# Optimization experiments

Hardware: AMD Instinct MI355X
Metric: run time of the kernel (lower is better)

## Reference

```python
import jax, jax.numpy as jnp
import numpy as np

H, D = 8, 16          # heads, per-head dim (hidden 128 = H*D)
IN_C, HID, OUT_C = 128, 128, 64
NG, ND = 100000, 50000
EG, EDG = 800000, 800000
NEG_SLOPE = 0.2


def setup_inputs() -> dict:
    key = jax.random.key(0)
    ks = jax.random.split(key, 20)
    inp = {}
    inp['x_gene'] = jax.random.normal(ks[0], (NG, IN_C), jnp.float32)
    inp['x_disease'] = jax.random.normal(ks[1], (ND, IN_C), jnp.float32)
    inp['eg_src'] = jax.random.randint(ks[2], (EG,), 0, NG, jnp.int32)
    inp['eg_dst'] = jax.random.randint(ks[3], (EG,), 0, NG, jnp.int32)
    inp['edg_src'] = jax.random.randint(ks[4], (EDG,), 0, ND, jnp.int32)
    inp['edg_dst'] = jax.random.randint(ks[5], (EDG,), 0, NG, jnp.int32)
    s = 1.0 / np.sqrt(IN_C)
    inp['W_gene'] = jax.random.normal(ks[6], (IN_C, HID), jnp.float32) * s
    inp['b_gene'] = jnp.zeros((HID,), jnp.float32)
    inp['W_dis'] = jax.random.normal(ks[7], (IN_C, HID), jnp.float32) * s
    inp['b_dis'] = jnp.zeros((HID,), jnp.float32)
    inp['att_src_gg'] = jax.random.normal(ks[8], (H, D), jnp.float32) * 0.1
    inp['att_dst_gg'] = jax.random.normal(ks[9], (H, D), jnp.float32) * 0.1
    inp['att_src_dg'] = jax.random.normal(ks[10], (H, D), jnp.float32) * 0.1
    inp['att_dst_dg'] = jax.random.normal(ks[11], (H, D), jnp.float32) * 0.1
    inp['Wk'] = jax.random.normal(ks[12], (HID, HID), jnp.float32) * (1.0 / np.sqrt(HID))
    inp['bk'] = jnp.zeros((HID,), jnp.float32)
    inp['q'] = jax.random.normal(ks[13], (HID,), jnp.float32) * 0.1
    inp['W_lin'] = jax.random.normal(ks[14], (HID, OUT_C), jnp.float32) * (1.0 / np.sqrt(HID))
    inp['b_lin'] = jnp.zeros((OUT_C,), jnp.float32)
    return inp


def _edge_attn(xs, xd, src, dst, a_s, a_d, n_dst):
    # xs:[Ns,H,D] projected src feats, xd:[Nd,H,D]; GAT-style per-edge-type attention
    e_src = (xs * a_s).sum(-1)                      # [Ns,H]
    e_dst = (xd * a_d).sum(-1)                      # [Nd,H]
    alpha = jax.nn.leaky_relu(e_src[src] + e_dst[dst], NEG_SLOPE)   # [E,H]
    m = jax.ops.segment_max(alpha, dst, num_segments=n_dst)
    m = jnp.where(jnp.isfinite(m), m, 0.0)
    ex = jnp.exp(alpha - m[dst])
    denom = jax.ops.segment_sum(ex, dst, num_segments=n_dst)
    w = ex / (denom[dst] + 1e-16)                   # softmax over incoming edges
    msg = xs[src] * w[..., None]                    # [E,H,D]
    out = jax.ops.segment_sum(msg, dst, num_segments=n_dst)  # [Nd,H,D]
    return jax.nn.relu(out.reshape(n_dst, H * D))


def reference(x_gene, x_disease, eg_src, eg_dst, edg_src, edg_dst,
              W_gene, b_gene, W_dis, b_dis,
              att_src_gg, att_dst_gg, att_src_dg, att_dst_dg,
              Wk, bk, q, W_lin, b_lin):
    ng = x_gene.shape[0]
    hg = (x_gene @ W_gene + b_gene).reshape(ng, H, D)
    hd = (x_disease @ W_dis + b_dis).reshape(-1, H, D)
    # metapath aggregations landing on 'gene'
    out_gg = _edge_attn(hg, hg, eg_src, eg_dst, att_src_gg, att_dst_gg, ng)
    out_dg = _edge_attn(hd, hg, edg_src, edg_dst, att_src_dg, att_dst_dg, ng)
    outs = jnp.stack([out_gg, out_dg])              # [K=2, Ng, HID]
    # semantic-level attention
    score = (jnp.tanh(outs @ Wk + bk).mean(1) * q).sum(-1)   # [K]
    beta = jax.nn.softmax(score)
    gene = (beta[:, None, None] * outs).sum(0)      # [Ng, HID]
    return gene @ W_lin + b_lin                     # [Ng, OUT_C]
```

## Files before the change

kernel.cpp:

```cpp
#include <hip/hip_runtime.h>
#include <cstdint>
#include <cstddef>

#define NEG_SLOPE 0.2f
#define BSHIFT 8

__device__ __forceinline__ float leakyf(float x) { return x > 0.f ? x : NEG_SLOPE * x; }
__device__ __forceinline__ float fast_tanh(float x) {
    float e = __expf(2.f * x);
    return 1.f - 2.f / (e + 1.f);
}

__global__ __launch_bounds__(256) void proj_kernel(
    const float* __restrict__ x, const float* __restrict__ W, const float* __restrict__ bias,
    float* __restrict__ hout, int N,
    const float* __restrict__ att0, float* __restrict__ e0,
    const float* __restrict__ att1, float* __restrict__ e1,
    const float* __restrict__ att2, float* __restrict__ e2)
{
    __shared__ float xlds[32 * 128];
    __shared__ float wlds[16 * 128];
    const int t = threadIdx.x;
    const int row0 = blockIdx.x * 32;
    #pragma unroll
    for (int p = 0; p < 4; ++p) {
        int idx = t + 256 * p;
        int r = idx >> 5;
        int c4 = idx & 31;
        float4 v = make_float4(0.f, 0.f, 0.f, 0.f);
        if (row0 + r < N) v = *(const float4*)(x + (size_t)(row0 + r) * 128 + c4 * 4);
        *(float4*)(xlds + r * 128 + c4 * 4) = v;
    }
    const int rg = t >> 5, ct = t & 31;
    float acc[4][4];
    {
        float4 bv = *(const float4*)(bias + ct * 4);
        #pragma unroll
        for (int rr = 0; rr < 4; ++rr) {
            acc[rr][0] = bv.x; acc[rr][1] = bv.y; acc[rr][2] = bv.z; acc[rr][3] = bv.w;
        }
    }
    for (int kc = 0; kc < 8; ++kc) {
        __syncthreads();
        #pragma unroll
        for (int p = 0; p < 2; ++p) {
            int idx = t + 256 * p;
            *(float4*)(wlds + idx * 4) = *(const float4*)(W + (size_t)kc * 2048 + idx * 4);
        }
        __syncthreads();
        #pragma unroll 2
        for (int i2 = 0; i2 < 16; i2 += 4) {
            const int i = kc * 16 + i2;
            float4 xv[4];
            #pragma unroll
            for (int rr = 0; rr < 4; ++rr) xv[rr] = *(const float4*)(xlds + (rg + 8 * rr) * 128 + i);
            #pragma unroll
            for (int qq = 0; qq < 4; ++qq) {
                float4 wv = *(const float4*)(wlds + (i2 + qq) * 128 + ct * 4);
                #pragma unroll
                for (int rr = 0; rr < 4; ++rr) {
                    float xs = ((const float*)&xv[rr])[qq];
                    acc[rr][0] = fmaf(xs, wv.x, acc[rr][0]);
                    acc[rr][1] = fmaf(xs, wv.y, acc[rr][1]);
                    acc[rr][2] = fmaf(xs, wv.z, acc[rr][2]);
                    acc[rr][3] = fmaf(xs, wv.w, acc[rr][3]);
                }
            }
        }
    }
    #pragma unroll
    for (int rr = 0; rr < 4; ++rr) {
        int grow = row0 + rg + 8 * rr;
        if (grow < N)
            *(float4*)(hout + (size_t)grow * 128 + ct * 4) =
                make_float4(acc[rr][0], acc[rr][1], acc[rr][2], acc[rr][3]);
    }
    const int head = ct >> 2;
    const bool wlane = (ct & 3) == 0;
    if (att0) {
        float4 av = *(const float4*)(att0 + ct * 4);
        #pragma unroll
        for (int rr = 0; rr < 4; ++rr) {
            float p_ = acc[rr][0] * av.x + acc[rr][1] * av.y + acc[rr][2] * av.z + acc[rr][3] * av.w;
            p_ += __shfl_xor(p_, 1);
            p_ += __shfl_xor(p_, 2);
            int grow = row0 + rg + 8 * rr;
            if (wlane && grow < N) e0[(size_t)grow * 8 + head] = p_;
        }
    }
    if (att1) {
        float4 av = *(const float4*)(att1 + ct * 4);
        #pragma unroll
        for (int rr = 0; rr < 4; ++rr) {
            float p_ = acc[rr][0] * av.x + acc[rr][1] * av.y + acc[rr][2] * av.z + acc[rr][3] * av.w;
            p_ += __shfl_xor(p_, 1);
            p_ += __shfl_xor(p_, 2);
            int grow = row0 + rg + 8 * rr;
            if (wlane && grow < N) e1[(size_t)grow * 8 + head] = p_;
        }
    }
    if (att2) {
        float4 av = *(const float4*)(att2 + ct * 4);
        #pragma unroll
        for (int rr = 0; rr < 4; ++rr) {
            float p_ = acc[rr][0] * av.x + acc[rr][1] * av.y + acc[rr][2] * av.z + acc[rr][3] * av.w;
            p_ += __shfl_xor(p_, 1);
            p_ += __shfl_xor(p_, 2);
            int grow = row0 + rg + 8 * rr;
            if (wlane && grow < N) e2[(size_t)grow * 8 + head] = p_;
        }
    }
}


__global__ __launch_bounds__(256) void bucket_hist(
    const int* __restrict__ dstg, int Eg, const int* __restrict__ dstd, int Ed,
    int NBg, int NBtot, int* __restrict__ bucketCnt)
{
    __shared__ int h[1024];
    const int t = threadIdx.x;
    for (int j = t; j < NBtot; j += 256) h[j] = 0;
    __syncthreads();
    const int Etot = Eg + Ed;
    const int base = blockIdx.x * 4096;
    #pragma unroll
    for (int k = 0; k < 16; ++k) {
        int i = base + k * 256 + t;
        if (i < Etot) {
            int b = (i < Eg) ? (dstg[i] >> BSHIFT) : NBg + (dstd[i - Eg] >> BSHIFT);
            atomicAdd(&h[b], 1);
        }
    }
    __syncthreads();
    for (int j = t; j < NBtot; j += 256) {
        int c = h[j];
        if (c) atomicAdd(&bucketCnt[j], c);
    }
}

__global__ void bucket_scan(const int* __restrict__ bucketCnt, int NBtot, int Etot,
                            int* __restrict__ bucketBase, int* __restrict__ bucketCursor)
{
    __shared__ int s[1024];
    int t = threadIdx.x;
    int v = (t < NBtot) ? bucketCnt[t] : 0;
    s[t] = v;
    __syncthreads();
    for (int o = 1; o < 1024; o <<= 1) {
        int add = (t >= o) ? s[t - o] : 0;
        __syncthreads();
        s[t] += add;
        __syncthreads();
    }
    if (t < NBtot) {
        int e = s[t] - v;
        bucketBase[t] = e;
        bucketCursor[t] = e;
    }
    if (t == 0) bucketBase[NBtot] = Etot;
}

__global__ __launch_bounds__(256) void bucket_scatter(
    const int* __restrict__ dstg, const int* __restrict__ srcg, int Eg,
    const int* __restrict__ dstd, const int* __restrict__ srcd, int Ed,
    int NBg, int NBtot, int* __restrict__ bucketCursor, unsigned* __restrict__ coarse)
{
    __shared__ int h[800];
    __shared__ int basearr[800];
    __shared__ int cur[800];
    const int t = threadIdx.x;
    for (int j = t; j < NBtot; j += 256) h[j] = 0;
    __syncthreads();
    const int Etot = Eg + Ed;
    const int base = blockIdx.x * 4096;
    int bk[16];
    unsigned pk[16];
    #pragma unroll
    for (int k = 0; k < 16; ++k) {
        int i = base + k * 256 + t;
        bk[k] = -1;
        if (i < Etot) {
            int dst, src, goff;
            if (i < Eg) { dst = dstg[i]; src = srcg[i]; goff = 0; }
            else        { dst = dstd[i - Eg]; src = srcd[i - Eg]; goff = NBg; }
            bk[k] = goff + (dst >> BSHIFT);
            pk[k] = (unsigned)src | ((unsigned)(dst & 255) << 24);
            atomicAdd(&h[bk[k]], 1);
        }
    }
    __syncthreads();
    for (int j = t; j < NBtot; j += 256) {
        int c = h[j];
        basearr[j] = c ? atomicAdd(&bucketCursor[j], c) : 0;
        cur[j] = 0;
    }
    __syncthreads();
    #pragma unroll
    for (int k = 0; k < 16; ++k) {
        if (bk[k] >= 0) {
            int r = atomicAdd(&cur[bk[k]], 1);
            coarse[basearr[bk[k]] + r] = pk[k];
        }
    }
}

__global__ __launch_bounds__(256) void bucket_sort(
    const unsigned* __restrict__ coarse, const int* __restrict__ bucketBase,
    int NBg, int Eg, int Ed, int N,
    int* __restrict__ offg, int* __restrict__ offd,
    int* __restrict__ srcs_g, int* __restrict__ srcs_d)
{
    __shared__ int hist[256];
    __shared__ int excl[256];
    __shared__ int cur[256];
    const int b = blockIdx.x;
    const int t = threadIdx.x;
    const int s0 = bucketBase[b], s1 = bucketBase[b + 1];
    const int cnt = s1 - s0;
    const bool isg = b < NBg;
    const int d0 = (isg ? b : b - NBg) << BSHIFT;
    hist[t] = 0;
    __syncthreads();
    for (int i = t; i < cnt; i += 256) {
        unsigned p = coarse[s0 + i];
        atomicAdd(&hist[p >> 24], 1);
    }
    __syncthreads();
    int v = hist[t];
    excl[t] = v;
    __syncthreads();
    for (int o = 1; o < 256; o <<= 1) {
        int add = (t >= o) ? excl[t - o] : 0;
        __syncthreads();
        excl[t] += add;
        __syncthreads();
    }
    const int e = excl[t] - v;
    const int localBase = isg ? s0 : s0 - Eg;
    const int d = d0 + t;
    if (d < N) {
        if (isg) offg[d] = localBase + e;
        else     offd[d] = localBase + e;
    }
    cur[t] = e;
    __syncthreads();
    int* outp = isg ? srcs_g : srcs_d;
    for (int i = t; i < cnt; i += 256) {
        unsigned p = coarse[s0 + i];
        int r = atomicAdd(&cur[p >> 24], 1);
        outp[localBase + r] = (int)(p & 0xFFFFFFu);
    }
    if (b == 0 && t == 0) { offg[N] = Eg; offd[N] = Ed; }
}

__global__ __launch_bounds__(256) void aggregate_kernel(
    const float* __restrict__ xs,
    const float* __restrict__ esrc,
    const float* __restrict__ edst,
    const int* __restrict__ off,
    const int* __restrict__ srcsorted,
    float* __restrict__ outp,
    int Nd)
{
    __shared__ float exbuf[4][64 * 8];
    const int lane = threadIdx.x & 63;
    const int wslot = threadIdx.x >> 6;
    const int n = blockIdx.x * 4 + wslot;
    if (n >= Nd) return;
    const int o0 = off[n], o1 = off[n + 1];
    const int deg = o1 - o0;
    const int li = lane & 31, half = lane >> 5;
    const int j0 = li * 4;
    const int hh = li >> 2;
    if (deg == 0) {
        if (half == 0) *(float4*)(outp + (size_t)n * 128 + j0) = make_float4(0.f, 0.f, 0.f, 0.f);
        return;
    }
    float ed[8];
    {
        float4 a = *(const float4*)(edst + (size_t)n * 8);
        float4 b = *(const float4*)(edst + (size_t)n * 8 + 4);
        ed[0] = a.x; ed[1] = a.y; ed[2] = a.z; ed[3] = a.w;
        ed[4] = b.x; ed[5] = b.y; ed[6] = b.z; ed[7] = b.w;
    }
    if (deg <= 64) {
        const bool act = lane < deg;
        int s = act ? srcsorted[o0 + lane] : 0;
        float m[8];
        {
            float4 ea = make_float4(0.f, 0.f, 0.f, 0.f), eb = ea;
            if (act) {
                ea = *(const float4*)(esrc + (size_t)s * 8);
                eb = *(const float4*)(esrc + (size_t)s * 8 + 4);
            }
            float a[8] = {ea.x, ea.y, ea.z, ea.w, eb.x, eb.y, eb.z, eb.w};
            #pragma unroll
            for (int h2 = 0; h2 < 8; ++h2) m[h2] = act ? leakyf(a[h2] + ed[h2]) : -1e30f;
        }
        float al[8];
        #pragma unroll
        for (int h2 = 0; h2 < 8; ++h2) al[h2] = m[h2];
        for (int o = 1; o < deg; o <<= 1) {
            #pragma unroll
            for (int h2 = 0; h2 < 8; ++h2) m[h2] = fmaxf(m[h2], __shfl_xor(m[h2], o));
        }
        float exv[8];
        #pragma unroll
        for (int h2 = 0; h2 < 8; ++h2) exv[h2] = act ? __expf(al[h2] - m[h2]) : 0.f;
        *(float4*)(&exbuf[wslot][lane * 8])     = make_float4(exv[0], exv[1], exv[2], exv[3]);
        *(float4*)(&exbuf[wslot][lane * 8 + 4]) = make_float4(exv[4], exv[5], exv[6], exv[7]);
        float4 num = make_float4(0.f, 0.f, 0.f, 0.f);
        float den = 0.f;
        const int iters = (deg + 1) >> 1;
        #pragma unroll 2
        for (int k = 0; k < iters; ++k) {
            int i = 2 * k + half;
            if (i < deg) {
                int si = __shfl(s, i);
                float wgt = exbuf[wslot][i * 8 + hh];
                float4 xv = *(const float4*)(xs + (size_t)si * 128 + j0);
                num.x = fmaf(wgt, xv.x, num.x);
                num.y = fmaf(wgt, xv.y, num.y);
                num.z = fmaf(wgt, xv.z, num.z);
                num.w = fmaf(wgt, xv.w, num.w);
                den += wgt;
            }
        }
        num.x += __shfl_xor(num.x, 32);
        num.y += __shfl_xor(num.y, 32);
        num.z += __shfl_xor(num.z, 32);
        num.w += __shfl_xor(num.w, 32);
        den += __shfl_xor(den, 32);
        if (half == 0) {
            float inv = 1.f / (den + 1e-16f);
            float4 r;
            r.x = fmaxf(num.x * inv, 0.f);
            r.y = fmaxf(num.y * inv, 0.f);
            r.z = fmaxf(num.z * inv, 0.f);
            r.w = fmaxf(num.w * inv, 0.f);
            *(float4*)(outp + (size_t)n * 128 + j0) = r;
        }
        return;
    }
    {
        const int j0b = lane * 2;
        const int h = lane >> 3;
        float m[8];
        #pragma unroll
        for (int hh2 = 0; hh2 < 8; ++hh2) m[hh2] = -1e30f;
        for (int base = 0; base < deg; base += 64) {
            int ii = base + lane;
            bool act = ii < deg;
            int s = srcsorted[o0 + (act ? ii : 0)];
            float4 ea = *(const float4*)(esrc + (size_t)s * 8);
            float4 eb = *(const float4*)(esrc + (size_t)s * 8 + 4);
            float a[8] = {ea.x, ea.y, ea.z, ea.w, eb.x, eb.y, eb.z, eb.w};
            #pragma unroll
            for (int hh2 = 0; hh2 < 8; ++hh2) {
                float v = act ? leakyf(a[hh2] + ed[hh2]) : -1e30f;
                #pragma unroll
                for (int o = 1; o < 64; o <<= 1) v = fmaxf(v, __shfl_xor(v, o));
                m[hh2] = fmaxf(m[hh2], v);
            }
        }
        float mh, edh;
        {
            float t4a = (h & 4) ? m[4] : m[0];
            float t4b = (h & 4) ? m[5] : m[1];
            float t4c = (h & 4) ? m[6] : m[2];
            float t4d = (h & 4) ? m[7] : m[3];
            float t2a = (h & 2) ? t4c : t4a;
            float t2b = (h & 2) ? t4d : t4b;
            mh = (h & 1) ? t2b : t2a;
            float u4a = (h & 4) ? ed[4] : ed[0];
            float u4b = (h & 4) ? ed[5] : ed[1];
            float u4c = (h & 4) ? ed[6] : ed[2];
            float u4d = (h & 4) ? ed[7] : ed[3];
            float u2a = (h & 2) ? u4c : u4a;
            float u2b = (h & 2) ? u4d : u4b;
            edh = (h & 1) ? u2b : u2a;
        }
        float den = 0.f, num0 = 0.f, num1 = 0.f;
        for (int base = 0; base < deg; base += 64) {
            int ii = base + lane;
            bool act = ii < deg;
            int sreg = srcsorted[o0 + (act ? ii : 0)];
            int cl = deg - base;
            if (cl > 64) cl = 64;
            for (int i = 0; i < cl; ++i) {
                int s = __shfl(sreg, i);
                float ev = esrc[(size_t)s * 8 + h];
                float ex = __expf(leakyf(ev + edh) - mh);
                float2 xv = *(const float2*)(xs + (size_t)s * 128 + j0b);
                num0 = fmaf(ex, xv.x, num0);
                num1 = fmaf(ex, xv.y, num1);
                den += ex;
            }
        }
        float inv = 1.f / (den + 1e-16f);
        float r0 = num0 * inv, r1 = num1 * inv;
        r0 = r0 > 0.f ? r0 : 0.f;
        r1 = r1 > 0.f ? r1 : 0.f;
        *(float2*)(outp + (size_t)n * 128 + j0b) = make_float2(r0, r1);
    }
}

__global__ __launch_bounds__(256) void score2_kernel(
    const float* __restrict__ gg, const float* __restrict__ dg,
    const float* __restrict__ Wk, const float* __restrict__ bk, const float* __restrict__ q,
    float* __restrict__ scoreAcc, int N)
{
    __shared__ float tile[32 * 128];
    __shared__ float wlds[16 * 128];
    __shared__ float sred[8];
    const int t = threadIdx.x;
    const int row0 = blockIdx.x * 16;
    #pragma unroll
    for (int p = 0; p < 4; ++p) {
        int idx = t + 256 * p;
        int r = idx >> 5;
        int c4 = idx & 31;
        int gr = row0 + (r & 15);
        const float* srcp = (r < 16) ? gg : dg;
        float4 v = make_float4(0.f, 0.f, 0.f, 0.f);
        if (gr < N) v = *(const float4*)(srcp + (size_t)gr * 128 + c4 * 4);
        *(float4*)(tile + r * 128 + c4 * 4) = v;
    }
    const int rg = t >> 5, ct = t & 31;
    float acc[4][4];
    {
        float4 bv = *(const float4*)(bk + ct * 4);
        #pragma unroll
        for (int rr = 0; rr < 4; ++rr) {
            acc[rr][0] = bv.x; acc[rr][1] = bv.y; acc[rr][2] = bv.z; acc[rr][3] = bv.w;
        }
    }
    for (int kc = 0; kc < 8; ++kc) {
        __syncthreads();
        #pragma unroll
        for (int p = 0; p < 2; ++p) {
            int idx = t + 256 * p;
            *(float4*)(wlds + idx * 4) = *(const float4*)(Wk + (size_t)kc * 2048 + idx * 4);
        }
        __syncthreads();
        #pragma unroll 2
        for (int i2 = 0; i2 < 16; i2 += 4) {
            const int i = kc * 16 + i2;
            float4 xv[4];
            #pragma unroll
            for (int rr = 0; rr < 4; ++rr) xv[rr] = *(const float4*)(tile + (rg + 8 * rr) * 128 + i);
            #pragma unroll
            for (int qq = 0; qq < 4; ++qq) {
                float4 wv = *(const float4*)(wlds + (i2 + qq) * 128 + ct * 4);
                #pragma unroll
                for (int rr = 0; rr < 4; ++rr) {
                    float xs = ((const float*)&xv[rr])[qq];
                    acc[rr][0] = fmaf(xs, wv.x, acc[rr][0]);
                    acc[rr][1] = fmaf(xs, wv.y, acc[rr][1]);
                    acc[rr][2] = fmaf(xs, wv.z, acc[rr][2]);
                    acc[rr][3] = fmaf(xs, wv.w, acc[rr][3]);
                }
            }
        }
    }
    float4 qv = *(const float4*)(q + ct * 4);
    float pg = 0.f, pd = 0.f;
    #pragma unroll
    for (int rr = 0; rr < 4; ++rr) {
        int r = rg + 8 * rr;
        int grow = row0 + (r & 15);
        if (grow < N) {
            float p_ = 0.f;
            p_ = fmaf(fast_tanh(acc[rr][0]), qv.x, p_);
            p_ = fmaf(fast_tanh(acc[rr][1]), qv.y, p_);
            p_ = fmaf(fast_tanh(acc[rr][2]), qv.z, p_);
            p_ = fmaf(fast_tanh(acc[rr][3]), qv.w, p_);
            if (r < 16) pg += p_; else pd += p_;
        }
    }
    #pragma unroll
    for (int o = 1; o < 64; o <<= 1) {
        pg += __shfl_xor(pg, o);
        pd += __shfl_xor(pd, o);
    }
    if ((t & 63) == 0) {
        sred[(t >> 6) * 2] = pg;
        sred[(t >> 6) * 2 + 1] = pd;
    }
    __syncthreads();
    if (t == 0) {
        float sg = sred[0] + sred[2] + sred[4] + sred[6];
        float sd = sred[1] + sred[3] + sred[5] + sred[7];
        int slot = blockIdx.x & 63;
        atomicAdd(&scoreAcc[slot], sg);
        atomicAdd(&scoreAcc[64 + slot], sd);
    }
}

__global__ void beta_kernel(float* __restrict__ scoreAcc, float invN) {
    int t = threadIdx.x;
    float v0 = scoreAcc[t];
    float v1 = scoreAcc[64 + t];
    #pragma unroll
    for (int o = 1; o < 64; o <<= 1) {
        v0 += __shfl_xor(v0, o);
        v1 += __shfl_xor(v1, o);
    }
    if (t == 0) {
        float s0 = v0 * invN, s1 = v1 * invN;
        float mx = fmaxf(s0, s1);
        float e0 = __expf(s0 - mx), e1 = __expf(s1 - mx);
        float inv = 1.f / (e0 + e1);
        scoreAcc[128] = e0 * inv;
        scoreAcc[129] = e1 * inv;
    }
}

__global__ __launch_bounds__(256) void final_kernel(
    const float* __restrict__ gg, const float* __restrict__ dg,
    const float* __restrict__ beta,
    const float* __restrict__ Wl, const float* __restrict__ bl,
    float* __restrict__ outp, int N)
{
    __shared__ float wlds[128 * 64];
    __shared__ float glds[32 * 128];
    const int t = threadIdx.x;
    #pragma unroll
    for (int p = 0; p < 8; ++p) {
        int idx = (t + 256 * p) * 4;
        *(float4*)(wlds + idx) = *(const float4*)(Wl + idx);
    }
    const float bet0 = beta[0], bet1 = beta[1];
    const int row0 = blockIdx.x * 32;
    #pragma unroll
    for (int p = 0; p < 4; ++p) {
        int idx = t + 256 * p;
        int r = idx >> 5;
        int c4 = idx & 31;
        float4 a = make_float4(0.f, 0.f, 0.f, 0.f), b = a, g;
        if (row0 + r < N) {
            a = *(const float4*)(gg + (size_t)(row0 + r) * 128 + c4 * 4);
            b = *(const float4*)(dg + (size_t)(row0 + r) * 128 + c4 * 4);
        }
        g.x = bet0 * a.x + bet1 * b.x;
        g.y = bet0 * a.y + bet1 * b.y;
        g.z = bet0 * a.z + bet1 * b.z;
        g.w = bet0 * a.w + bet1 * b.w;
        *(float4*)(glds + r * 128 + c4 * 4) = g;
    }
    __syncthreads();
    const int rg = t >> 5, ct = t & 31;
    float acc[4][2];
    {
        float2 bv = *(const float2*)(bl + ct * 2);
        #pragma unroll
        for (int rr = 0; rr < 4; ++rr) { acc[rr][0] = bv.x; acc[rr][1] = bv.y; }
    }
    #pragma unroll 2
    for (int i = 0; i < 128; i += 4) {
        float4 xv[4];
        #pragma unroll
        for (int rr = 0; rr < 4; ++rr) xv[rr] = *(const float4*)(glds + (rg + 8 * rr) * 128 + i);
        #pragma unroll
        for (int qq = 0; qq < 4; ++qq) {
            float2 wv = *(const float2*)(wlds + (i + qq) * 64 + ct * 2);
            #pragma unroll
            for (int rr = 0; rr < 4; ++rr) {
                float xs = ((const float*)&xv[rr])[qq];
                acc[rr][0] = fmaf(xs, wv.x, acc[rr][0]);
                acc[rr][1] = fmaf(xs, wv.y, acc[rr][1]);
            }
        }
    }
    #pragma unroll
    for (int rr = 0; rr < 4; ++rr) {
        int grow = row0 + rg + 8 * rr;
        if (grow < N)
            *(float2*)(outp + (size_t)grow * 64 + ct * 2) = make_float2(acc[rr][0], acc[rr][1]);
    }
}

extern "C" void kernel_launch(void* const* d_in, const int* in_sizes, int n_in,
                              void* d_out, int out_size, void* d_ws, size_t ws_size,
                              hipStream_t stream) {
    (void)n_in; (void)out_size; (void)ws_size;
    const float* x_gene = (const float*)d_in[0];
    const float* x_dis  = (const float*)d_in[1];
    const int* eg_src   = (const int*)d_in[2];
    const int* eg_dst   = (const int*)d_in[3];
    const int* edg_src  = (const int*)d_in[4];
    const int* edg_dst  = (const int*)d_in[5];
    const float* W_gene = (const float*)d_in[6];
    const float* b_gene = (const float*)d_in[7];
    const float* W_dis  = (const float*)d_in[8];
    const float* b_dis  = (const float*)d_in[9];
    const float* att_src_gg = (const float*)d_in[10];
    const float* att_dst_gg = (const float*)d_in[11];
    const float* att_src_dg = (const float*)d_in[12];
    const float* att_dst_dg = (const float*)d_in[13];
    const float* Wk    = (const float*)d_in[14];
    const float* bk    = (const float*)d_in[15];
    const float* q     = (const float*)d_in[16];
    const float* W_lin = (const float*)d_in[17];
    const float* b_lin = (const float*)d_in[18];
    float* out = (float*)d_out;

    const int NG_ = in_sizes[0] / 128;
    const int ND_ = in_sizes[1] / 128;
    const int EG_ = in_sizes[2];
    const int EDG_ = in_sizes[4];

    char* w = (char*)d_ws;
    auto alloc = [&](size_t bytes) -> char* {
        char* p = w;
        w += (bytes + 255) & ~(size_t)255;
        return p;
    };
    float* hg       = (float*)alloc((size_t)NG_ * 128 * 4);
    float* hd       = (float*)alloc((size_t)ND_ * 128 * 4);
    float* e_src_gg = (float*)alloc((size_t)NG_ * 8 * 4);
    float* e_dst_gg = (float*)alloc((size_t)NG_ * 8 * 4);
    float* e_dst_dg = (float*)alloc((size_t)NG_ * 8 * 4);
    float* e_src_dg = (float*)alloc((size_t)ND_ * 8 * 4);
    float* out_gg   = (float*)alloc((size_t)NG_ * 128 * 4);
    int* offg  = (int*)alloc((size_t)(NG_ + 1) * 4);
    int* offd  = (int*)alloc((size_t)(NG_ + 1) * 4);
    int* srcs_g = (int*)alloc((size_t)EG_ * 4);
    int* srcs_d = (int*)alloc((size_t)EDG_ * 4);
    unsigned* coarse = (unsigned*)alloc((size_t)(EG_ + EDG_) * 4);
    int* bucketCnt    = (int*)alloc(4096);
    int* bucketBase   = (int*)alloc(4096);
    int* bucketCursor = (int*)alloc(4096);
    float* score = (float*)alloc(1024);
    float* out_dg = hg;

    const int NBg = (NG_ + 255) >> BSHIFT;
    const int NBtot = 2 * NBg;
    const int Etot = EG_ + EDG_;
    const int nbE = (Etot + 4095) / 4096;

    proj_kernel<<<(NG_ + 31) / 32, 256, 0, stream>>>(
        x_gene, W_gene, b_gene, hg, NG_,
        att_src_gg, e_src_gg, att_dst_gg, e_dst_gg, att_dst_dg, e_dst_dg);
    proj_kernel<<<(ND_ + 31) / 32, 256, 0, stream>>>(
        x_dis, W_dis, b_dis, hd, ND_,
        att_src_dg, e_src_dg, (const float*)nullptr, (float*)nullptr,
        (const float*)nullptr, (float*)nullptr);

    hipMemsetAsync(bucketCnt, 0, (size_t)NBtot * 4, stream);
    bucket_hist<<<nbE, 256, 0, stream>>>(eg_dst, EG_, edg_dst, EDG_, NBg, NBtot, bucketCnt);
    bucket_scan<<<1, 1024, 0, stream>>>(bucketCnt, NBtot, Etot, bucketBase, bucketCursor);
    bucket_scatter<<<nbE, 256, 0, stream>>>(
        eg_dst, eg_src, EG_, edg_dst, edg_src, EDG_, NBg, NBtot, bucketCursor, coarse);
    bucket_sort<<<NBtot, 256, 0, stream>>>(
        coarse, bucketBase, NBg, EG_, EDG_, NG_, offg, offd, srcs_g, srcs_d);

    aggregate_kernel<<<(NG_ + 3) / 4, 256, 0, stream>>>(
        hg, e_src_gg, e_dst_gg, offg, srcs_g, out_gg, NG_);
    aggregate_kernel<<<(NG_ + 3) / 4, 256, 0, stream>>>(
        hd, e_src_dg, e_dst_dg, offd, srcs_d, out_dg, NG_);

    hipMemsetAsync(score, 0, 512, stream);
    score2_kernel<<<(NG_ + 15) / 16, 256, 0, stream>>>(out_gg, out_dg, Wk, bk, q, score, NG_);
    beta_kernel<<<1, 64, 0, stream>>>(score, 1.0f / (float)NG_);

    final_kernel<<<(NG_ + 31) / 32, 256, 0, stream>>>(
        out_gg, out_dg, score + 128, W_lin, b_lin, out, NG_);
}
```

Before: 427.0 us.

## Compute semantic attention scores with bf16 MFMA instead of FP32 FMA

Replaces the FP32 scalar-FMA score kernel with one that converts the 64 output rows per block (32 from each metapath) to bf16 in swizzled LDS and multiplies them by a pre-transposed bf16 Wk using 16x16x32 MFMA instructions, then applies bias, tanh and q. A small kernel transposes and converts Wk to bf16 once per call. This moves the Ng x 128 x 128 matmul onto matrix cores and halves the block count, at the cost of bf16 rounding in the score that feeds the softmax beta.

```diff
diff --git a/kernel.cpp b/kernel.cpp
--- a/kernel.cpp
+++ b/kernel.cpp
@@ -4,11 +4,19 @@
 
 #define NEG_SLOPE 0.2f
 #define BSHIFT 8
+
+typedef __attribute__((ext_vector_type(8))) short short8;
+typedef __attribute__((ext_vector_type(4))) float f32x4;
 
 __device__ __forceinline__ float leakyf(float x) { return x > 0.f ? x : NEG_SLOPE * x; }
 __device__ __forceinline__ float fast_tanh(float x) {
     float e = __expf(2.f * x);
     return 1.f - 2.f / (e + 1.f);
+}
+__device__ __forceinline__ unsigned short f2bf(float x) {
+    unsigned u = __float_as_uint(x);
+    unsigned r = u + 0x7FFFu + ((u >> 16) & 1u);
+    return (unsigned short)(r >> 16);
 }
 
 __global__ __launch_bounds__(256) void proj_kernel(
@@ -112,7 +120,6 @@
     }
 }
 
-
 __global__ __launch_bounds__(256) void bucket_hist(
     const int* __restrict__ dstg, int Eg, const int* __restrict__ dstd, int Ed,
     int NBg, int NBtot, int* __restrict__ bucketCnt)
@@ -405,95 +412,86 @@
     }
 }
 
-__global__ __launch_bounds__(256) void score2_kernel(
+__global__ void wkt_kernel(const float* __restrict__ Wk, unsigned short* __restrict__ WkT) {
+    int c = threadIdx.x;
+    for (int k = 0; k < 128; ++k)
+        WkT[c * 128 + k] = f2bf(Wk[(size_t)k * 128 + c]);
+}
+
+__global__ __launch_bounds__(256) void score2_mfma(
     const float* __restrict__ gg, const float* __restrict__ dg,
-    const float* __restrict__ Wk, const float* __restrict__ bk, const float* __restrict__ q,
+    const unsigned short* __restrict__ WkT,
+    const float* __restrict__ bk, const float* __restrict__ q,
     float* __restrict__ scoreAcc, int N)
 {
-    __shared__ float tile[32 * 128];
-    __shared__ float wlds[16 * 128];
-    __shared__ float sred[8];
+    __shared__ short atile[64 * 128];
+    __shared__ float sred[4];
     const int t = threadIdx.x;
-    const int row0 = blockIdx.x * 16;
-    #pragma unroll
-    for (int p = 0; p < 4; ++p) {
-        int idx = t + 256 * p;
-        int r = idx >> 5;
-        int c4 = idx & 31;
-        int gr = row0 + (r & 15);
-        const float* srcp = (r < 16) ? gg : dg;
-        float4 v = make_float4(0.f, 0.f, 0.f, 0.f);
-        if (gr < N) v = *(const float4*)(srcp + (size_t)gr * 128 + c4 * 4);
-        *(float4*)(tile + r * 128 + c4 * 4) = v;
-    }
-    const int rg = t >> 5, ct = t & 31;
-    float acc[4][4];
+    const int row0 = blockIdx.x * 32;
     {
-        float4 bv = *(const float4*)(bk + ct * 4);
-        #pragma unroll
-        for (int rr = 0; rr < 4; ++rr) {
-            acc[rr][0] = bv.x; acc[rr][1] = bv.y; acc[rr][2] = bv.z; acc[rr][3] = bv.w;
-        }
-    }
-    for (int kc = 0; kc < 8; ++kc) {
-        __syncthreads();
-        #pragma unroll
-        for (int p = 0; p < 2; ++p) {
-            int idx = t + 256 * p;
-            *(float4*)(wlds + idx * 4) = *(const float4*)(Wk + (size_t)kc * 2048 + idx * 4);
-        }
-        __syncthreads();
-        #pragma unroll 2
-        for (int i2 = 0; i2 < 16; i2 += 4) {
-            const int i = kc * 16 + i2;
-            float4 xv[4];
-            #pragma unroll
-            for (int rr = 0; rr < 4; ++rr) xv[rr] = *(const float4*)(tile + (rg + 8 * rr) * 128 + i);
-            #pragma unroll
-            for (int qq = 0; qq < 4; ++qq) {
-                float4 wv = *(const float4*)(wlds + (i2 + qq) * 128 + ct * 4);
-                #pragma unroll
-                for (int rr = 0; rr < 4; ++rr) {
-                    float xs = ((const float*)&xv[rr])[qq];
-                    acc[rr][0] = fmaf(xs, wv.x, acc[rr][0]);
-                    acc[rr][1] = fmaf(xs, wv.y, acc[rr][1]);
-                    acc[rr][2] = fmaf(xs, wv.z, acc[rr][2]);
-                    acc[rr][3] = fmaf(xs, wv.w, acc[rr][3]);
-                }
+        const int row = t >> 2, q4 = t & 3;
+        const int gr = row0 + (row & 31);
+        const float* srcp = (row < 32) ? gg : dg;
+        #pragma unroll
+        for (int c = 0; c < 4; ++c) {
+            const int kc = q4 * 4 + c;
+            float4 l0 = make_float4(0.f, 0.f, 0.f, 0.f), l1 = l0;
+            if (gr < N) {
+                l0 = *(const float4*)(srcp + (size_t)gr * 128 + kc * 8);
+                l1 = *(const float4*)(srcp + (size_t)gr * 128 + kc * 8 + 4);
             }
-        }
-    }
-    float4 qv = *(const float4*)(q + ct * 4);
-    float pg = 0.f, pd = 0.f;
-    #pragma unroll
-    for (int rr = 0; rr < 4; ++rr) {
-        int r = rg + 8 * rr;
-        int grow = row0 + (r & 15);
-        if (grow < N) {
-            float p_ = 0.f;
-            p_ = fmaf(fast_tanh(acc[rr][0]), qv.x, p_);
-            p_ = fmaf(fast_tanh(acc[rr][1]), qv.y, p_);
-            p_ = fmaf(fast_tanh(acc[rr][2]), qv.z, p_);
-            p_ = fmaf(fast_tanh(acc[rr][3]), qv.w, p_);
-            if (r < 16) pg += p_; else pd += p_;
-        }
-    }
-    #pragma unroll
-    for (int o = 1; o < 64; o <<= 1) {
-        pg += __shfl_xor(pg, o);
-        pd += __shfl_xor(pd, o);
-    }
-    if ((t & 63) == 0) {
-        sred[(t >> 6) * 2] = pg;
-        sred[(t >> 6) * 2 + 1] = pd;
-    }
+            int4 u;
+            u.x = (int)f2bf(l0.x) | ((int)f2bf(l0.y) << 16);
+            u.y = (int)f2bf(l0.z) | ((int)f2bf(l0.w) << 16);
+            u.z = (int)f2bf(l1.x) | ((int)f2bf(l1.y) << 16);
+            u.w = (int)f2bf(l1.z) | ((int)f2bf(l1.w) << 16);
+            const int chunk = row * 16 + kc;
+            const int chunk_sw = chunk ^ (row & 7);
+            *(int4*)((char*)atile + chunk_sw * 16) = u;
+        }
+    }
+    __syncthreads();
+    const int w = t >> 6, l = t & 63;
+    const int lrow = l & 15, lk = l >> 4;
+    f32x4 acc[8];
+    #pragma unroll
+    for (int ct = 0; ct < 8; ++ct) { acc[ct][0] = 0.f; acc[ct][1] = 0.f; acc[ct][2] = 0.f; acc[ct][3] = 0.f; }
+    #pragma unroll
+    for (int ks = 0; ks < 4; ++ks) {
+        const int rowl = w * 16 + lrow;
+        const int chunk = rowl * 16 + ks * 4 + lk;
+        const int chunk_sw = chunk ^ (rowl & 7);
+        short8 afr = *(short8*)((char*)atile + chunk_sw * 16);
+        #pragma unroll
+        for (int ct = 0; ct < 8; ++ct) {
+            const unsigned short* bp = WkT + ((size_t)(ct * 16 + lrow) * 128 + ks * 32 + lk * 8);
+            short8 bfr = *(const short8*)bp;
+            acc[ct] = __builtin_amdgcn_mfma_f32_16x16x32_bf16(afr, bfr, acc[ct], 0, 0, 0);
+        }
+    }
+    float s = 0.f;
+    #pragma unroll
+    for (int ct = 0; ct < 8; ++ct) {
+        const int col = ct * 16 + lrow;
+        const float bkv = bk[col];
+        const float qv = q[col];
+        #pragma unroll
+        for (int r = 0; r < 4; ++r) {
+            const int rloc = lk * 4 + r;
+            const int grow = row0 + ((w * 16 + rloc) & 31);
+            if (grow < N) s = fmaf(fast_tanh(acc[ct][r] + bkv), qv, s);
+        }
+    }
+    #pragma unroll
+    for (int o = 1; o < 64; o <<= 1) s += __shfl_xor(s, o);
+    if (l == 0) sred[w] = s;
     __syncthreads();
     if (t == 0) {
-        float sg = sred[0] + sred[2] + sred[4] + sred[6];
-        float sd = sred[1] + sred[3] + sred[5] + sred[7];
+        float pg = sred[0] + sred[1];
+        float pd = sred[2] + sred[3];
         int slot = blockIdx.x & 63;
-        atomicAdd(&scoreAcc[slot], sg);
-        atomicAdd(&scoreAcc[64 + slot], sd);
+        atomicAdd(&scoreAcc[slot], pg);
+        atomicAdd(&scoreAcc[64 + slot], pd);
     }
 }
 
@@ -631,6 +629,7 @@
     int* bucketCnt    = (int*)alloc(4096);
     int* bucketBase   = (int*)alloc(4096);
     int* bucketCursor = (int*)alloc(4096);
+    unsigned short* WkT = (unsigned short*)alloc(128 * 128 * 2);
     float* score = (float*)alloc(1024);
     float* out_dg = hg;
 
@@ -646,6 +645,7 @@
         x_dis, W_dis, b_dis, hd, ND_,
         att_src_dg, e_src_dg, (const float*)nullptr, (float*)nullptr,
         (const float*)nullptr, (float*)nullptr);
+    wkt_kernel<<<1, 128, 0, stream>>>(Wk, WkT);
 
     hipMemsetAsync(bucketCnt, 0, (size_t)NBtot * 4, stream);
     bucket_hist<<<nbE, 256, 0, stream>>>(eg_dst, EG_, edg_dst, EDG_, NBg, NBtot, bucketCnt);
@@ -661,7 +661,7 @@
         hd, e_src_dg, e_dst_dg, offd, srcs_d, out_dg, NG_);
 
     hipMemsetAsync(score, 0, 512, stream);
-    score2_kernel<<<(NG_ + 15) / 16, 256, 0, stream>>>(out_gg, out_dg, Wk, bk, q, score, NG_);
+    score2_mfma<<<(NG_ + 31) / 32, 256, 0, stream>>>(out_gg, out_dg, WkT, bk, q, score, NG_);
     beta_kernel<<<1, 64, 0, stream>>>(score, 1.0f / (float)NG_);
 
     final_kernel<<<(NG_ + 31) / 32, 256, 0, stream>>>(
```

Result: no change. 419.1 us (-1.8%).
